# Kernel tuning notes

Hardware: AMD Instinct MI355X
Metric: run time of the kernel (lower is better)

The kernel has to match this reference:

```python
import jax, jax.numpy as jnp
import numpy as np

B0, L0, C0 = 4, 576, 256
DST, DCONV, EXP = 48, 4, 2
DIN = EXP * C0          # 512 internal dim
DTR = C0 // 16          # 16 delta rank
FD = 2 * C0             # 512 ffn dim (mlp_ratio=2)


def setup_inputs() -> dict:
    key = jax.random.key(0)
    ks = iter(jax.random.split(key, 32))
    def n(shape, s=0.02):
        return jax.random.normal(next(ks), shape, dtype=jnp.float32) * s
    return {
        'x': jax.random.normal(next(ks), (B0, L0, C0), dtype=jnp.float32),
        'ln1_g': jnp.ones((C0,), jnp.float32), 'ln1_b': jnp.zeros((C0,), jnp.float32),
        'mln_g': jnp.ones((C0,), jnp.float32), 'mln_b': jnp.zeros((C0,), jnp.float32),
        'w_in': n((C0, DIN * EXP)),
        'conv_w': n((DCONV, DIN)), 'conv_b': jnp.zeros((DIN,), jnp.float32),
        'w_xproj': n((DIN, DTR + 2 * DST)),
        'w_dt': n((DTR, DIN)), 'b_dt': jnp.zeros((DIN,), jnp.float32),
        'A_log': jnp.log(jnp.tile(jnp.arange(1, DST + 1, dtype=jnp.float32), (DIN, 1))),
        'D': jnp.ones((DIN,), jnp.float32),
        'w_out': n((DIN, C0)),
        'ln2_g': jnp.ones((C0,), jnp.float32), 'ln2_b': jnp.zeros((C0,), jnp.float32),
        'fc1_w': n((C0, FD)), 'bn1_s': jnp.ones((FD,), jnp.float32), 'bn1_b': jnp.zeros((FD,), jnp.float32),
        'Wr': n((FD, FD)), 'Wi': n((FD, FD)), 'rb': n((FD,)), 'ib': n((FD,)),
        'fc2_w': n((FD, C0)), 'bn2_s': jnp.ones((C0,), jnp.float32), 'bn2_b': jnp.zeros((C0,), jnp.float32),
    }


def _ln(x, g, b, eps=1e-3):
    m = jnp.mean(x, -1, keepdims=True)
    v = jnp.mean((x - m) ** 2, -1, keepdims=True)
    return (x - m) / jnp.sqrt(v + eps) * g + b


def _selective_scan(u, delta, A, Bm, Cm, D):
    # u,delta:[b,l,d]; A:[d,n]; Bm,Cm:[b,l,n]; D:[d]
    dA = jnp.einsum('bld,dn->bldn', delta, A)
    dB_u = jnp.einsum('bld,bld,bln->bldn', delta, u, Bm)
    shifted = jnp.pad(dA[:, 1:], ((0, 0), (1, 1), (0, 0), (0, 0)))[:, 1:]
    dA_cumsum = jnp.exp(jnp.cumsum(shifted[:, ::-1], axis=1))[:, ::-1]
    xs = jnp.cumsum(dB_u * dA_cumsum, axis=1) / (dA_cumsum + 1e-12)
    y = jnp.einsum('bldn,bln->bld', xs, Cm)
    return y + u * D


def _forward(x, ln1_g, ln1_b, mln_g, mln_b, w_in, conv_w, conv_b, w_xproj, w_dt, b_dt,
             A_log, D, w_out, ln2_g, ln2_b, fc1_w, bn1_s, bn1_b, Wr, Wi, rb, ib,
             fc2_w, bn2_s, bn2_b):
    # ---- Mamba branch: x + Mamba(LN_mamba(LN1(x))) ----
    h = _ln(_ln(x, ln1_g, ln1_b), mln_g, mln_b)
    xr = h @ w_in                                   # [b,l,4C]
    xm, res = xr[..., :DIN], xr[..., DIN:]
    # causal depthwise conv1d (pad left k-1)
    xp = jnp.pad(xm, ((0, 0), (DCONV - 1, 0), (0, 0)))
    xc = jax.lax.conv_general_dilated(
        xp, conv_w[:, None, :], (1,), 'VALID',
        dimension_numbers=('NLC', 'LIO', 'NLC'), feature_group_count=DIN) + conv_b
    xc = jax.nn.silu(xc)
    A = -jnp.exp(A_log)
    x_dbl = xc @ w_xproj
    dt, Bm, Cm = x_dbl[..., :DTR], x_dbl[..., DTR:DTR + DST], x_dbl[..., DTR + DST:]
    delta = jax.nn.softplus(dt @ w_dt + b_dt)
    y = _selective_scan(xc, delta, A, Bm, Cm, D)
    y = y * jax.nn.silu(res)
    x = x + y @ w_out
    # ---- Frequency-domain FFN branch: x + FFN(LN2(x)) ----
    h2 = _ln(x, ln2_g, ln2_b)
    f = jax.nn.relu((h2 @ fc1_w) * bn1_s + bn1_b)   # fc1 (1x1 conv) + BN(eval) + ReLU
    L = f.shape[1]
    scale = L ** 0.5
    fr = jnp.fft.rfft(f, axis=1)                    # fft over sequence length
    real, imag = fr.real / scale, fr.imag / scale
    xre = jax.nn.relu(jnp.einsum('bnc,cd->bnd', real, Wr) - jnp.einsum('bnc,cd->bnd', imag, Wi) + rb)
    xim = jax.nn.relu(jnp.einsum('bnc,cd->bnd', imag, Wr) + jnp.einsum('bnc,cd->bnd', real, Wi) + ib)
    ff = jnp.fft.irfft((xre + 1j * xim) * scale, n=L, axis=1)
    out2 = (ff @ fc2_w) * bn2_s + bn2_b             # fc2 (1x1 conv) + BN(eval)
    return x + out2


def reference(x, ln1_g, ln1_b, mln_g, mln_b, w_in, conv_w, conv_b, w_xproj, w_dt, b_dt,
              A_log, D, w_out, ln2_g, ln2_b, fc1_w, bn1_s, bn1_b, Wr, Wi, rb, ib,
              fc2_w, bn2_s, bn2_b):
    return _forward(x, ln1_g, ln1_b, mln_g, mln_b, w_in, conv_w, conv_b, w_xproj, w_dt,
                    b_dt, A_log, D, w_out, ln2_g, ln2_b, fc1_w, bn1_s, bn1_b, Wr, Wi,
                    rb, ib, fc2_w, bn2_s, bn2_b)
```

## Files before the change

kernel.cpp:

```cpp
#include <hip/hip_runtime.h>
#include <math.h>

#define NB 4
#define NL 576
#define NC 256
#define NTOK (NB*NL)
#define NDIN 512
#define NXD 112
#define NDTR 16
#define NDST 48
#define NFREQ 289
#define NWIN 1024
#define NMROW (NB*NFREQ)
#define NKPK 608

#define OFF_HB    0u
#define OFF_XRF   147456u
#define OFF_XCT   2506752u
#define OFF_REST  3686400u
#define OFF_XCB   4866048u
#define OFF_XDBL  5455872u
#define OFF_YFT   5584896u
#define OFF_X2    6764544u
#define OFF_FTB   7354368u
#define OFF_RF    7944192u
#define OFF_IF    8240128u
#define OFF_YFB   8536064u
#define OFF_FFB   9125888u
#define OFF_WINT  9715712u
#define OFF_WRT   9846784u
#define OFF_WIT   9977856u
#define OFF_WXPT  10108928u
#define OFF_WOT   10137600u
#define OFF_FC1T  10203136u
#define OFF_FC2T  10268672u
#define OFF_CF    10334208u
#define OFF_SF    10426368u
#define OFF_CI    10518528u

typedef __attribute__((ext_vector_type(8))) short bf16x8;
typedef __attribute__((ext_vector_type(4))) float f32x4;
typedef __attribute__((ext_vector_type(4))) int   i32x4;

__device__ __forceinline__ float wave_sum(float v) {
#pragma unroll
  for (int o = 32; o > 0; o >>= 1) v += __shfl_xor(v, o);
  return v;
}

__device__ __forceinline__ unsigned short f2bf(float f) {
  unsigned int u = __float_as_uint(f);
  unsigned int r = (u + 0x7fffu + ((u >> 16) & 1u)) >> 16;
  return (unsigned short)r;
}
__device__ __forceinline__ float b2f(unsigned short u) {
  return __uint_as_float(((unsigned int)u) << 16);
}

__device__ __forceinline__ float wave_iscan(float x, int lane) {
  x += __int_as_float(__builtin_amdgcn_update_dpp(0, __float_as_int(x), 0x111, 0xf, 0xf, true));
  x += __int_as_float(__builtin_amdgcn_update_dpp(0, __float_as_int(x), 0x112, 0xf, 0xf, true));
  x += __int_as_float(__builtin_amdgcn_update_dpp(0, __float_as_int(x), 0x114, 0xf, 0xf, true));
  x += __int_as_float(__builtin_amdgcn_update_dpp(0, __float_as_int(x), 0x118, 0xf, 0xf, true));
  int xi = __float_as_int(x);
  float s15 = __int_as_float(__builtin_amdgcn_readlane(xi, 15));
  float s31 = __int_as_float(__builtin_amdgcn_readlane(xi, 31));
  float s47 = __int_as_float(__builtin_amdgcn_readlane(xi, 47));
  float off = 0.f;
  if (lane >= 16) off += s15;
  if (lane >= 32) off += s31;
  if (lane >= 48) off += s47;
  return x + off;
}

__device__ void packT_dev(const float* __restrict__ src, unsigned short* __restrict__ dst,
                          int R, int C, int tile, int cblks) {
  __shared__ float t[64][65];
  int cb = tile % cblks, rb = tile / cblks;
  int c0 = cb * 64, r0 = rb * 64;
  int tid = threadIdx.x;
  for (int u = tid; u < 4096; u += 256) {
    int r = u >> 6, c = u & 63;
    float v = 0.f;
    if (r0 + r < R && c0 + c < C) v = src[(size_t)(r0 + r) * C + c0 + c];
    t[r][c] = v;
  }
  __syncthreads();
  for (int u = tid; u < 4096; u += 256) {
    int nr = u >> 6, nc = u & 63;
    if (c0 + nr < C && r0 + nc < R)
      dst[(size_t)(c0 + nr) * R + r0 + nc] = f2bf(t[nc][nr]);
  }
}

__global__ __launch_bounds__(256) void setup_kernel(
    const float* __restrict__ w_in, const float* __restrict__ Wr,
    const float* __restrict__ Wi, const float* __restrict__ wxp,
    const float* __restrict__ wo, const float* __restrict__ fc1,
    const float* __restrict__ fc2,
    unsigned short* __restrict__ winT, unsigned short* __restrict__ Wrt,
    unsigned short* __restrict__ Wit, unsigned short* __restrict__ wxpT,
    unsigned short* __restrict__ woT, unsigned short* __restrict__ fc1T,
    unsigned short* __restrict__ fc2T, unsigned short* __restrict__ Cf,
    unsigned short* __restrict__ Sf, unsigned short* __restrict__ Ci) {
  int bid = blockIdx.x;
  const float TWO_PI_N = 6.28318530717958647692f / (float)NL;
  if (bid < 64)       packT_dev(w_in, winT, NC, NWIN, bid, 16);
  else if (bid < 128) packT_dev(Wr, Wrt, NDIN, NDIN, bid - 64, 8);
  else if (bid < 192) packT_dev(Wi, Wit, NDIN, NDIN, bid - 128, 8);
  else if (bid < 208) packT_dev(wxp, wxpT, NDIN, NXD, bid - 192, 2);
  else if (bid < 240) packT_dev(wo, woT, NDIN, NC, bid - 208, 4);
  else if (bid < 272) packT_dev(fc1, fc1T, NC, NDIN, bid - 240, 8);
  else if (bid < 304) packT_dev(fc2, fc2T, NDIN, NC, bid - 272, 4);
  else if (bid < 384) {
    int m0 = (bid - 304) * 4;
    for (int u = threadIdx.x; u < 4 * NL; u += 256) {
      int m = m0 + u / NL, l = u % NL;
      float c = 0.f, s = 0.f;
      if (m < NFREQ) {
        int idx = (m * l) % NL;
        float sv, cv;
        __sincosf(TWO_PI_N * idx, &sv, &cv);
        c = cv * (1.f / 24.f);
        s = -sv * (1.f / 24.f);
      }
      Cf[(size_t)m * NL + l] = f2bf(c);
      Sf[(size_t)m * NL + l] = f2bf(s);
    }
  } else {
    int l0 = (bid - 384) * 8;
    for (int u = threadIdx.x; u < 8 * NKPK; u += 256) {
      int l = l0 + u / NKPK, k = u % NKPK;
      float v = 0.f;
      if (k < NFREQ) {
        float w = (k == 0 || k == NFREQ - 1) ? 1.f : 2.f;
        int idx = (k * l) % NL;
        float sv, cv;
        __sincosf(TWO_PI_N * idx, &sv, &cv);
        v = w * cv * (1.f / 24.f);
      } else if (k < 2 * NFREQ) {
        int kk = k - NFREQ;
        float w = (kk == 0 || kk == NFREQ - 1) ? 1.f : 2.f;
        int idx = (kk * l) % NL;
        float sv, cv;
        __sincosf(TWO_PI_N * idx, &sv, &cv);
        v = -w * sv * (1.f / 24.f);
      }
      Ci[(size_t)l * NKPK + k] = f2bf(v);
    }
  }
}

__global__ void ln_kernel(const float* __restrict__ in, unsigned short* __restrict__ out,
                          const float* __restrict__ g1, const float* __restrict__ b1,
                          const float* __restrict__ g2, const float* __restrict__ b2,
                          int dbl) {
  int row = blockIdx.x, lane = threadIdx.x;
  const float* p = in + (size_t)row * NC;
  float v[4];
#pragma unroll
  for (int j = 0; j < 4; ++j) v[j] = p[lane + j * 64];
  float s = wave_sum(v[0] + v[1] + v[2] + v[3]);
  float m = s * (1.f / NC);
  float q = 0.f;
#pragma unroll
  for (int j = 0; j < 4; ++j) { float d = v[j] - m; q += d * d; }
  q = wave_sum(q);
  float rs = 1.f / sqrtf(q * (1.f / NC) + 1e-3f);
#pragma unroll
  for (int j = 0; j < 4; ++j) {
    int c = lane + j * 64;
    v[j] = (v[j] - m) * rs * g1[c] + b1[c];
  }
  if (dbl) {
    s = wave_sum(v[0] + v[1] + v[2] + v[3]);
    m = s * (1.f / NC);
    q = 0.f;
#pragma unroll
    for (int j = 0; j < 4; ++j) { float d = v[j] - m; q += d * d; }
    q = wave_sum(q);
    rs = 1.f / sqrtf(q * (1.f / NC) + 1e-3f);
#pragma unroll
    for (int j = 0; j < 4; ++j) {
      int c = lane + j * 64;
      v[j] = (v[j] - m) * rs * g2[c] + b2[c];
    }
  }
  unsigned short* o = out + (size_t)row * NC;
#pragma unroll
  for (int j = 0; j < 4; ++j) o[lane + j * 64] = f2bf(v[j]);
}

__global__ __launch_bounds__(256) void packT_kernel(
    const float* __restrict__ src, unsigned short* __restrict__ dst, int R, int C) {
  packT_dev(src, dst, R, C, blockIdx.y * gridDim.x + blockIdx.x, gridDim.x);
}

__global__ __launch_bounds__(256) void gemm_mfma(
    const unsigned short* __restrict__ A, const unsigned short* __restrict__ B,
    void* __restrict__ C, int ldc, int M, int N, int K, int mode, int flags,
    const float* __restrict__ scl, const float* __restrict__ bias,
    const float* __restrict__ add, int ldadd) {
  __shared__ unsigned short As[64][40], Bs[64][40];
  int tid = threadIdx.x, lane = tid & 63, wv = tid >> 6;
  int n0 = blockIdx.x * 64, m0 = blockIdx.y * 64;
  int sm = tid >> 2, part = tid & 3;
  f32x4 acc[4] = {};
  for (int k0 = 0; k0 < K; k0 += 32) {
    *(bf16x8*)&As[sm][part * 8] = *(const bf16x8*)(A + (size_t)(m0 + sm) * K + k0 + part * 8);
    bf16x8 bv = {};
    if (n0 + sm < N) bv = *(const bf16x8*)(B + (size_t)(n0 + sm) * K + k0 + part * 8);
    *(bf16x8*)&Bs[sm][part * 8] = bv;
    __syncthreads();
    int am = wv * 16 + (lane & 15), koff = (lane >> 4) * 8;
    bf16x8 a = *(bf16x8*)&As[am][koff];
#pragma unroll
    for (int t = 0; t < 4; ++t) {
      bf16x8 b = *(bf16x8*)&Bs[t * 16 + (lane & 15)][koff];
      acc[t] = __builtin_amdgcn_mfma_f32_16x16x32_bf16(a, b, acc[t], 0, 0, 0);
    }
    __syncthreads();
  }
#pragma unroll
  for (int t = 0; t < 4; ++t) {
    int gn = n0 + t * 16 + (lane & 15);
    if (gn >= N) continue;
    float sv = scl ? scl[gn] : 0.f, bvv = bias ? bias[gn] : 0.f;
#pragma unroll
    for (int r = 0; r < 4; ++r) {
      int gm = m0 + wv * 16 + (lane >> 4) * 4 + r;
      float v = acc[t][r];
      if (mode == 2) v += add[(size_t)gm * ldadd + gn];
      else if (mode == 3) v = fmaxf(v * sv + bvv, 0.f);
      else if (mode == 4) v = v * sv + bvv + add[(size_t)gm * ldadd + gn];
      int gms = gm;
      if (flags & 8) {
        int bq = gm / NL, tt = gm - bq * NL;
        int t9 = tt / 9;
        gms = bq * NL + (tt - t9 * 9) * 64 + t9;
      }
      size_t o = (flags & 2) ? (size_t)gn * ldc + gms : (size_t)gm * ldc + gn;
      if (flags & 4) ((unsigned short*)C)[o] = f2bf(v);
      else ((float*)C)[o] = v;
    }
  }
}

__global__ __launch_bounds__(256) void convT_kernel(
    const float* __restrict__ xr, const float* __restrict__ cw,
    const float* __restrict__ cb, float* __restrict__ xc_t,
    float* __restrict__ res_t, unsigned short* __restrict__ xcb) {
  __shared__ float tile[67][65];
  int d0 = blockIdx.x * 64;
  int rt = blockIdx.y;
  int b = rt / 9, l0 = (rt % 9) * 64;
  int tid = threadIdx.x;
  int li = tid & 63, dj0 = tid >> 6;
  if (blockIdx.z == 0) {
    for (int u = tid; u < 67 * 16; u += 256) {
      int r = u >> 4, c4 = (u & 15) * 4;
      int l = l0 - 3 + r;
      float4 v = make_float4(0.f, 0.f, 0.f, 0.f);
      if (l >= 0) v = *reinterpret_cast<const float4*>(xr + (size_t)(b * NL + l) * NWIN + d0 + c4);
      tile[r][c4 + 0] = v.x; tile[r][c4 + 1] = v.y;
      tile[r][c4 + 2] = v.z; tile[r][c4 + 3] = v.w;
    }
    __syncthreads();
    float outv[16];
#pragma unroll
    for (int k2 = 0; k2 < 16; ++k2) {
      int dj = dj0 + k2 * 4;
      int d = d0 + dj;
      float acc = cb[d];
#pragma unroll
      for (int k = 0; k < 4; ++k) acc += cw[k * NDIN + d] * tile[li + k][dj];
      acc = acc / (1.f + __expf(-acc));
      outv[k2] = acc;
      xc_t[(size_t)d * NTOK + b * NL + l0 + li] = acc;
    }
    __syncthreads();
#pragma unroll
    for (int k2 = 0; k2 < 16; ++k2) tile[li][dj0 + k2 * 4] = outv[k2];
    __syncthreads();
    for (int u = tid; u < 1024; u += 256) {
      int r = u >> 4, c4 = (u & 15) * 4;
      unsigned long long pk =
          (unsigned long long)f2bf(tile[r][c4 + 0]) |
          ((unsigned long long)f2bf(tile[r][c4 + 1]) << 16) |
          ((unsigned long long)f2bf(tile[r][c4 + 2]) << 32) |
          ((unsigned long long)f2bf(tile[r][c4 + 3]) << 48);
      *(unsigned long long*)(xcb + (size_t)(b * NL + l0 + r) * NDIN + d0 + c4) = pk;
    }
  } else {
    for (int u = tid; u < 64 * 16; u += 256) {
      int r = u >> 4, c4 = (u & 15) * 4;
      float4 v = *reinterpret_cast<const float4*>(xr + (size_t)(b * NL + l0 + r) * NWIN + NDIN + d0 + c4);
      tile[r][c4 + 0] = v.x; tile[r][c4 + 1] = v.y;
      tile[r][c4 + 2] = v.z; tile[r][c4 + 3] = v.w;
    }
    __syncthreads();
    for (int dj = dj0; dj < 64; dj += 4)
      res_t[(size_t)(d0 + dj) * NTOK + b * NL + l0 + li] = tile[li][dj];
  }
}

__global__ __launch_bounds__(256) void scan7_kernel(
    const float* __restrict__ xc_t, const unsigned short* __restrict__ xdbl,
    const float* __restrict__ w_dt, const float* __restrict__ b_dt,
    const float* __restrict__ A_log, const float* __restrict__ Dp,
    const float* __restrict__ res_t, float* __restrict__ yf_t) {
  __shared__ float yl[4][NL];
  __shared__ float u_lds[NL];
  int b = blockIdx.x >> 9, d = blockIdx.x & 511;
  int tid = threadIdx.x, lane = tid & 63, wv = tid >> 6;
  int bbase = b * NL;
  const float* urow = xc_t + (size_t)d * NTOK;

  for (int e = tid; e < NL; e += 256) u_lds[e] = urow[bbase + e];

  float wdt[16];
#pragma unroll
  for (int r = 0; r < 16; ++r) wdt[r] = w_dt[r * NDIN + d];
  float bd = b_dt[d];
  float dl[9];
#pragma unroll
  for (int j = 0; j < 9; ++j) dl[j] = bd;
#pragma unroll
  for (int r = 0; r < 16; ++r) {
    const unsigned short* dtp = xdbl + (size_t)r * NTOK + bbase;
#pragma unroll
    for (int j = 0; j < 9; ++j) dl[j] += b2f(dtp[j * 64 + lane]) * wdt[r];
  }
#pragma unroll
  for (int j = 0; j < 9; ++j) {
    float v = dl[j];
    dl[j] = fmaxf(v, 0.f) + __logf(1.f + __expf(-fabsf(v)));
  }
  __syncthreads();

  float ul[9];
#pragma unroll
  for (int j = 0; j < 9; ++j) ul[j] = u_lds[lane * 9 + j];
  float pre[9];
  float s = 0.f;
#pragma unroll
  for (int j = 0; j < 9; ++j) { s += dl[j]; pre[j] = s; }
  float isc = wave_iscan(s, lane);
  float total = __int_as_float(__builtin_amdgcn_readlane(__float_as_int(isc), 63));
  float excl = isc - s;
  float Ts[9], dlul[9];
#pragma unroll
  for (int j = 0; j < 9; ++j) {
    Ts[j] = total - excl - pre[j];
    dlul[j] = dl[j] * ul[j];
  }

  const float* Arow = A_log + (size_t)d * NDST + wv * 12;
  float y[9] = {};
  for (int jj = 0; jj < 12; ++jj) {
    float An = -__expf(Arow[jj]);
    const unsigned short* bbp = xdbl + (size_t)(NDTR + wv * 12 + jj) * NTOK + bbase;
    const unsigned short* ccp = xdbl + (size_t)(NDTR + NDST + wv * 12 + jj) * NTOK + bbase;
    float e[9], w[9];
    float ps = 0.f;
#pragma unroll
    for (int j = 0; j < 9; ++j) {
      e[j] = __expf(An * Ts[j]);
      ps += dlul[j] * b2f(bbp[j * 64 + lane]) * e[j];
      w[j] = ps;
    }
    float wi = wave_iscan(ps, lane);
    float wexcl = wi - ps;
#pragma unroll
    for (int j = 0; j < 9; ++j)
      y[j] += __fdividef(w[j] + wexcl, e[j] + 1e-12f) * b2f(ccp[j * 64 + lane]);
  }
#pragma unroll
  for (int j = 0; j < 9; ++j) yl[wv][lane * 9 + j] = y[j];
  __syncthreads();

  const float* rrow = res_t + (size_t)d * NTOK;
  float* orow = yf_t + (size_t)d * NTOK;
  float Dd = Dp[d];
  for (int e0 = tid; e0 < NL; e0 += 256) {
    float yy = yl[0][e0] + yl[1][e0] + yl[2][e0] + yl[3][e0];
    float uu = u_lds[e0];
    float rr = rrow[bbase + e0];
    float yv = yy + uu * Dd;
    float sr = rr / (1.f + __expf(-rr));
    orow[bbase + e0] = yv * sr;
  }
}

__global__ __launch_bounds__(256) void dftf_mfma_kernel(
    const unsigned short* __restrict__ Cf, const unsigned short* __restrict__ Sf,
    const unsigned short* __restrict__ ft,
    unsigned short* __restrict__ RFb, unsigned short* __restrict__ IFb) {
  __shared__ unsigned short AsC[64][40], AsS[64][40], Bs[64][40];
  int tid = threadIdx.x;
  int lane = tid & 63, wv = tid >> 6;
  int n0 = blockIdx.x * 64, m0 = blockIdx.y * 64, b = blockIdx.z;
  int sm = tid >> 2, part = tid & 3;
  f32x4 accR[4] = {}, accI[4] = {};
  for (int k0 = 0; k0 < NL; k0 += 32) {
    *(bf16x8*)&AsC[sm][part * 8] = *(const bf16x8*)(Cf + (size_t)(m0 + sm) * NL + k0 + part * 8);
    *(bf16x8*)&AsS[sm][part * 8] = *(const bf16x8*)(Sf + (size_t)(m0 + sm) * NL + k0 + part * 8);
    *(bf16x8*)&Bs[sm][part * 8]  = *(const bf16x8*)(ft + (size_t)(n0 + sm) * NTOK + b * NL + k0 + part * 8);
    __syncthreads();
    int am = wv * 16 + (lane & 15);
    int koff = (lane >> 4) * 8;
    bf16x8 ac = *(bf16x8*)&AsC[am][koff];
    bf16x8 as = *(bf16x8*)&AsS[am][koff];
#pragma unroll
    for (int t = 0; t < 4; ++t) {
      bf16x8 bv = *(bf16x8*)&Bs[t * 16 + (lane & 15)][koff];
      accR[t] = __builtin_amdgcn_mfma_f32_16x16x32_bf16(ac, bv, accR[t], 0, 0, 0);
      accI[t] = __builtin_amdgcn_mfma_f32_16x16x32_bf16(as, bv, accI[t], 0, 0, 0);
    }
    __syncthreads();
  }
#pragma unroll
  for (int t = 0; t < 4; ++t) {
    int gn = n0 + t * 16 + (lane & 15);
#pragma unroll
    for (int r = 0; r < 4; ++r) {
      int gm = m0 + wv * 16 + (lane >> 4) * 4 + r;
      if (gm < NFREQ) {
        size_t o = ((size_t)(b * NFREQ + gm)) * NDIN + gn;
        RFb[o] = f2bf(accR[t][r]);
        IFb[o] = f2bf(accI[t][r]);
      }
    }
  }
}

__global__ __launch_bounds__(256) void mix_mfma_kernel(
    const unsigned short* __restrict__ RFb, const unsigned short* __restrict__ IFb,
    const unsigned short* __restrict__ Wrt, const unsigned short* __restrict__ Wit,
    const float* __restrict__ rb, const float* __restrict__ ib,
    unsigned short* __restrict__ PK) {
  __shared__ unsigned short AsR[64][40], AsI[64][40], BsR[64][40], BsI[64][40];
  int tid = threadIdx.x;
  int lane = tid & 63, wv = tid >> 6;
  int n0 = blockIdx.x * 64, m0 = blockIdx.y * 64;
  int sm = tid >> 2, part = tid & 3;
  f32x4 accR[4] = {}, accI[4] = {};
  for (int k0 = 0; k0 < NDIN; k0 += 32) {
    *(bf16x8*)&AsR[sm][part * 8] = *(const bf16x8*)(Wrt + (size_t)(m0 + sm) * NDIN + k0 + part * 8);
    *(bf16x8*)&AsI[sm][part * 8] = *(const bf16x8*)(Wit + (size_t)(m0 + sm) * NDIN + k0 + part * 8);
    bf16x8 brf = {}, bif = {};
    if (n0 + sm < NMROW) {
      brf = *(const bf16x8*)(RFb + (size_t)(n0 + sm) * NDIN + k0 + part * 8);
      bif = *(const bf16x8*)(IFb + (size_t)(n0 + sm) * NDIN + k0 + part * 8);
    }
    *(bf16x8*)&BsR[sm][part * 8] = brf;
    *(bf16x8*)&BsI[sm][part * 8] = bif;
    __syncthreads();
    int am = wv * 16 + (lane & 15);
    int koff = (lane >> 4) * 8;
    bf16x8 a_wr = *(bf16x8*)&AsR[am][koff];
    bf16x8 a_wi = *(bf16x8*)&AsI[am][koff];
    union { bf16x8 h; i32x4 i; } un;
    un.h = a_wi;
    un.i = un.i ^ (int)0x80008000;
    bf16x8 a_win = un.h;
#pragma unroll
    for (int t = 0; t < 4; ++t) {
      bf16x8 b_rf = *(bf16x8*)&BsR[t * 16 + (lane & 15)][koff];
      bf16x8 b_if = *(bf16x8*)&BsI[t * 16 + (lane & 15)][koff];
      accR[t] = __builtin_amdgcn_mfma_f32_16x16x32_bf16(a_wr, b_rf, accR[t], 0, 0, 0);
      accR[t] = __builtin_amdgcn_mfma_f32_16x16x32_bf16(a_win, b_if, accR[t], 0, 0, 0);
      accI[t] = __builtin_amdgcn_mfma_f32_16x16x32_bf16(a_wr, b_if, accI[t], 0, 0, 0);
      accI[t] = __builtin_amdgcn_mfma_f32_16x16x32_bf16(a_wi, b_rf, accI[t], 0, 0, 0);
    }
    __syncthreads();
  }
#pragma unroll
  for (int t = 0; t < 4; ++t) {
    int gn = n0 + t * 16 + (lane & 15);
    int bb = (gn >= 3 * NFREQ) ? 3 : (gn >= 2 * NFREQ) ? 2 : (gn >= NFREQ) ? 1 : 0;
    int kf = gn - bb * NFREQ;
    bool ok = gn < NMROW;
#pragma unroll
    for (int r = 0; r < 4; ++r) {
      int gm = m0 + wv * 16 + (lane >> 4) * 4 + r;
      if (ok) {
        float vr = fmaxf(accR[t][r] + rb[gm], 0.f);
        float vi = fmaxf(accI[t][r] + ib[gm], 0.f);
        size_t base = ((size_t)gm * NB + bb) * NKPK;
        PK[base + kf] = f2bf(vr);
        PK[base + NFREQ + kf] = f2bf(vi);
      }
    }
  }
}

__global__ __launch_bounds__(256) void idft_mfma_kernel(
    const unsigned short* __restrict__ Ci, const unsigned short* __restrict__ PK,
    unsigned short* __restrict__ ffb) {
  __shared__ unsigned short As[64][40], Bs[64][40];
  int tid = threadIdx.x;
  int lane = tid & 63, wv = tid >> 6;
  int n0 = blockIdx.x * 64, m0 = blockIdx.y * 64, b = blockIdx.z;
  int sm = tid >> 2, part = tid & 3;
  f32x4 acc[4] = {};
  for (int k0 = 0; k0 < NKPK; k0 += 32) {
    *(bf16x8*)&As[sm][part * 8] = *(const bf16x8*)(Ci + (size_t)(m0 + sm) * NKPK + k0 + part * 8);
    bf16x8 bv = *(const bf16x8*)(PK + ((size_t)(n0 + sm) * NB + b) * NKPK + k0 + part * 8);
    if (k0 + part * 8 >= 2 * NFREQ - 2) {
      union { bf16x8 h; i32x4 i; } u;
      u.h = bv;
      if (k0 + part * 8 == 576) { u.i[1] = 0; u.i[2] = 0; u.i[3] = 0; }
      else { u.i[0] = 0; u.i[1] = 0; u.i[2] = 0; u.i[3] = 0; }
      bv = u.h;
    }
    *(bf16x8*)&Bs[sm][part * 8] = bv;
    __syncthreads();
    int am = wv * 16 + (lane & 15);
    int koff = (lane >> 4) * 8;
    bf16x8 av = *(bf16x8*)&As[am][koff];
#pragma unroll
    for (int t = 0; t < 4; ++t) {
      bf16x8 b2 = *(bf16x8*)&Bs[t * 16 + (lane & 15)][koff];
      acc[t] = __builtin_amdgcn_mfma_f32_16x16x32_bf16(av, b2, acc[t], 0, 0, 0);
    }
    __syncthreads();
  }
#pragma unroll
  for (int t = 0; t < 4; ++t) {
    int gn = n0 + t * 16 + (lane & 15);
#pragma unroll
    for (int r = 0; r < 4; ++r) {
      int gm = m0 + wv * 16 + (lane >> 4) * 4 + r;
      ffb[((size_t)(b * NL + gm)) * NDIN + gn] = f2bf(acc[t][r]);
    }
  }
}

extern "C" void kernel_launch(void* const* d_in, const int* in_sizes, int n_in,
                              void* d_out, int out_size, void* d_ws, size_t ws_size,
                              hipStream_t stream) {
  const float* x      = (const float*)d_in[0];
  const float* ln1_g  = (const float*)d_in[1];
  const float* ln1_b  = (const float*)d_in[2];
  const float* mln_g  = (const float*)d_in[3];
  const float* mln_b  = (const float*)d_in[4];
  const float* w_in   = (const float*)d_in[5];
  const float* conv_w = (const float*)d_in[6];
  const float* conv_b = (const float*)d_in[7];
  const float* w_xprj = (const float*)d_in[8];
  const float* w_dt   = (const float*)d_in[9];
  const float* b_dt   = (const float*)d_in[10];
  const float* A_log  = (const float*)d_in[11];
  const float* Dp     = (const float*)d_in[12];
  const float* w_out  = (const float*)d_in[13];
  const float* ln2_g  = (const float*)d_in[14];
  const float* ln2_b  = (const float*)d_in[15];
  const float* fc1_w  = (const float*)d_in[16];
  const float* bn1_s  = (const float*)d_in[17];
  const float* bn1_b  = (const float*)d_in[18];
  const float* Wr     = (const float*)d_in[19];
  const float* Wi     = (const float*)d_in[20];
  const float* rb     = (const float*)d_in[21];
  const float* ib     = (const float*)d_in[22];
  const float* fc2_w  = (const float*)d_in[23];
  const float* bn2_s  = (const float*)d_in[24];
  const float* bn2_b  = (const float*)d_in[25];

  float* ws = (float*)d_ws;
  unsigned short* hb   = (unsigned short*)(ws + OFF_HB);
  float* xr     = ws + OFF_XRF;
  float* xc_t   = ws + OFF_XCT;
  float* res_t  = ws + OFF_REST;
  float* yf_t   = ws + OFF_YFT;
  float* x2     = ws + OFF_X2;
  unsigned short* xcb  = (unsigned short*)(ws + OFF_XCB);
  unsigned short* xdbl = (unsigned short*)(ws + OFF_XDBL);
  unsigned short* PK   = (unsigned short*)(ws + OFF_YFT);
  unsigned short* ftb  = (unsigned short*)(ws + OFF_FTB);
  unsigned short* RFb  = (unsigned short*)(ws + OFF_RF);
  unsigned short* IFb  = (unsigned short*)(ws + OFF_IF);
  unsigned short* yfb  = (unsigned short*)(ws + OFF_YFB);
  unsigned short* ffb  = (unsigned short*)(ws + OFF_FFB);
  unsigned short* winT = (unsigned short*)(ws + OFF_WINT);
  unsigned short* Wrt  = (unsigned short*)(ws + OFF_WRT);
  unsigned short* Wit  = (unsigned short*)(ws + OFF_WIT);
  unsigned short* wxpT = (unsigned short*)(ws + OFF_WXPT);
  unsigned short* woT  = (unsigned short*)(ws + OFF_WOT);
  unsigned short* fc1T = (unsigned short*)(ws + OFF_FC1T);
  unsigned short* fc2T = (unsigned short*)(ws + OFF_FC2T);
  unsigned short* Cfb  = (unsigned short*)(ws + OFF_CF);
  unsigned short* Sfb  = (unsigned short*)(ws + OFF_SF);
  unsigned short* Cib  = (unsigned short*)(ws + OFF_CI);
  unsigned short* h2b  = hb;
  float* out = (float*)d_out;

  setup_kernel<<<456, 256, 0, stream>>>(w_in, Wr, Wi, w_xprj, w_out, fc1_w, fc2_w,
                                        winT, Wrt, Wit, wxpT, woT, fc1T, fc2T,
                                        Cfb, Sfb, Cib);
  ln_kernel<<<NTOK, 64, 0, stream>>>(x, hb, ln1_g, ln1_b, mln_g, mln_b, 1);
  gemm_mfma<<<dim3(16, 36), 256, 0, stream>>>(hb, winT, xr, NWIN, NTOK, NWIN, NC,
                                              0, 0, nullptr, nullptr, nullptr, 0);
  convT_kernel<<<dim3(8, 36, 2), 256, 0, stream>>>(xr, conv_w, conv_b, xc_t, res_t, xcb);
  gemm_mfma<<<dim3(2, 36), 256, 0, stream>>>(xcb, wxpT, xdbl, NTOK, NTOK, NXD, NDIN,
                                             0, 14, nullptr, nullptr, nullptr, 0);
  scan7_kernel<<<NB * NDIN, 256, 0, stream>>>(xc_t, xdbl, w_dt, b_dt, A_log, Dp, res_t, yf_t);
  packT_kernel<<<dim3(36, 8), 256, 0, stream>>>(yf_t, yfb, NDIN, NTOK);
  gemm_mfma<<<dim3(4, 36), 256, 0, stream>>>(yfb, woT, x2, NC, NTOK, NC, NDIN,
                                             2, 0, nullptr, nullptr, x, NC);
  ln_kernel<<<NTOK, 64, 0, stream>>>(x2, h2b, ln2_g, ln2_b, nullptr, nullptr, 0);
  gemm_mfma<<<dim3(8, 36), 256, 0, stream>>>(h2b, fc1T, ftb, NTOK, NTOK, NDIN, NC,
                                             3, 6, bn1_s, bn1_b, nullptr, 0);
  dftf_mfma_kernel<<<dim3(8, 5, NB), 256, 0, stream>>>(Cfb, Sfb, ftb, RFb, IFb);
  mix_mfma_kernel<<<dim3(19, 8), 256, 0, stream>>>(RFb, IFb, Wrt, Wit, rb, ib, PK);
  idft_mfma_kernel<<<dim3(8, 9, NB), 256, 0, stream>>>(Cib, PK, ffb);
  gemm_mfma<<<dim3(4, 36), 256, 0, stream>>>(ffb, fc2T, out, NC, NTOK, NC, NDIN,
                                             4, 0, bn2_s, bn2_b, x2, NC);
}
```

Before: 186.2 us.

## Store in-proj, conv and residual intermediates as bf16 and restructure scan

The in-projection GEMM now writes bf16 output, and the conv/transposition kernel reads bf16 and writes the transposed conv activations and residual as bf16. This roughly halves the memory traffic of these intermediates between the GEMM, conv and scan kernels. The scan kernel computes delta cooperatively into shared memory across all threads instead of redundantly per wave. It also processes two state channels per iteration to expose more independent exp and scan work. The cost is reduced precision on u and the residual gate, plus extra shared memory and register pressure.

After: 199.9 us. 1.07x slower.

```diff
diff --git a/kernel.cpp b/kernel.cpp
--- a/kernel.cpp
+++ b/kernel.cpp
@@ -247,9 +247,9 @@
 }
 
 __global__ __launch_bounds__(256) void convT_kernel(
-    const float* __restrict__ xr, const float* __restrict__ cw,
-    const float* __restrict__ cb, float* __restrict__ xc_t,
-    float* __restrict__ res_t, unsigned short* __restrict__ xcb) {
+    const unsigned short* __restrict__ xrb, const float* __restrict__ cw,
+    const float* __restrict__ cb, unsigned short* __restrict__ xc_tb,
+    unsigned short* __restrict__ res_tb, unsigned short* __restrict__ xcb) {
   __shared__ float tile[67][65];
   int d0 = blockIdx.x * 64;
   int rt = blockIdx.y;
@@ -257,13 +257,17 @@
   int tid = threadIdx.x;
   int li = tid & 63, dj0 = tid >> 6;
   if (blockIdx.z == 0) {
-    for (int u = tid; u < 67 * 16; u += 256) {
-      int r = u >> 4, c4 = (u & 15) * 4;
+    for (int u = tid; u < 67 * 8; u += 256) {
+      int r = u >> 3, c8 = (u & 7) * 8;
       int l = l0 - 3 + r;
-      float4 v = make_float4(0.f, 0.f, 0.f, 0.f);
-      if (l >= 0) v = *reinterpret_cast<const float4*>(xr + (size_t)(b * NL + l) * NWIN + d0 + c4);
-      tile[r][c4 + 0] = v.x; tile[r][c4 + 1] = v.y;
-      tile[r][c4 + 2] = v.z; tile[r][c4 + 3] = v.w;
+      if (l >= 0) {
+        bf16x8 v = *(const bf16x8*)(xrb + (size_t)(b * NL + l) * NWIN + d0 + c8);
+#pragma unroll
+        for (int q = 0; q < 8; ++q) tile[r][c8 + q] = b2f((unsigned short)v[q]);
+      } else {
+#pragma unroll
+        for (int q = 0; q < 8; ++q) tile[r][c8 + q] = 0.f;
+      }
     }
     __syncthreads();
     float outv[16];
@@ -276,7 +280,7 @@
       for (int k = 0; k < 4; ++k) acc += cw[k * NDIN + d] * tile[li + k][dj];
       acc = acc / (1.f + __expf(-acc));
       outv[k2] = acc;
-      xc_t[(size_t)d * NTOK + b * NL + l0 + li] = acc;
+      xc_tb[(size_t)d * NTOK + b * NL + l0 + li] = f2bf(acc);
     }
     __syncthreads();
 #pragma unroll
@@ -292,55 +296,50 @@
       *(unsigned long long*)(xcb + (size_t)(b * NL + l0 + r) * NDIN + d0 + c4) = pk;
     }
   } else {
-    for (int u = tid; u < 64 * 16; u += 256) {
-      int r = u >> 4, c4 = (u & 15) * 4;
-      float4 v = *reinterpret_cast<const float4*>(xr + (size_t)(b * NL + l0 + r) * NWIN + NDIN + d0 + c4);
-      tile[r][c4 + 0] = v.x; tile[r][c4 + 1] = v.y;
-      tile[r][c4 + 2] = v.z; tile[r][c4 + 3] = v.w;
+    for (int u = tid; u < 64 * 8; u += 256) {
+      int r = u >> 3, c8 = (u & 7) * 8;
+      bf16x8 v = *(const bf16x8*)(xrb + (size_t)(b * NL + l0 + r) * NWIN + NDIN + d0 + c8);
+#pragma unroll
+      for (int q = 0; q < 8; ++q) tile[r][c8 + q] = b2f((unsigned short)v[q]);
     }
     __syncthreads();
     for (int dj = dj0; dj < 64; dj += 4)
-      res_t[(size_t)(d0 + dj) * NTOK + b * NL + l0 + li] = tile[li][dj];
-  }
-}
-
-__global__ __launch_bounds__(256) void scan7_kernel(
-    const float* __restrict__ xc_t, const unsigned short* __restrict__ xdbl,
+      res_tb[(size_t)(d0 + dj) * NTOK + b * NL + l0 + li] = f2bf(tile[li][dj]);
+  }
+}
+
+__global__ __launch_bounds__(256) void scan8_kernel(
+    const unsigned short* __restrict__ xc_tb, const unsigned short* __restrict__ xdbl,
     const float* __restrict__ w_dt, const float* __restrict__ b_dt,
     const float* __restrict__ A_log, const float* __restrict__ Dp,
-    const float* __restrict__ res_t, float* __restrict__ yf_t) {
+    const unsigned short* __restrict__ res_tb, float* __restrict__ yf_t) {
   __shared__ float yl[4][NL];
   __shared__ float u_lds[NL];
+  __shared__ float dl_lds[NL];
   int b = blockIdx.x >> 9, d = blockIdx.x & 511;
   int tid = threadIdx.x, lane = tid & 63, wv = tid >> 6;
   int bbase = b * NL;
-  const float* urow = xc_t + (size_t)d * NTOK;
-
-  for (int e = tid; e < NL; e += 256) u_lds[e] = urow[bbase + e];
-
+  const unsigned short* urow = xc_tb + (size_t)d * NTOK;
+
+  for (int e = tid; e < NL; e += 256) u_lds[e] = b2f(urow[bbase + e]);
   float wdt[16];
 #pragma unroll
   for (int r = 0; r < 16; ++r) wdt[r] = w_dt[r * NDIN + d];
   float bd = b_dt[d];
-  float dl[9];
-#pragma unroll
-  for (int j = 0; j < 9; ++j) dl[j] = bd;
-#pragma unroll
-  for (int r = 0; r < 16; ++r) {
-    const unsigned short* dtp = xdbl + (size_t)r * NTOK + bbase;
-#pragma unroll
-    for (int j = 0; j < 9; ++j) dl[j] += b2f(dtp[j * 64 + lane]) * wdt[r];
-  }
+  for (int p = tid; p < NL; p += 256) {
+    float v = bd;
+#pragma unroll
+    for (int r = 0; r < 16; ++r) v += b2f(xdbl[(size_t)r * NTOK + bbase + p]) * wdt[r];
+    dl_lds[p] = fmaxf(v, 0.f) + __logf(1.f + __expf(-fabsf(v)));
+  }
+  __syncthreads();
+
+  float dl[9], ul[9];
 #pragma unroll
   for (int j = 0; j < 9; ++j) {
-    float v = dl[j];
-    dl[j] = fmaxf(v, 0.f) + __logf(1.f + __expf(-fabsf(v)));
-  }
-  __syncthreads();
-
-  float ul[9];
-#pragma unroll
-  for (int j = 0; j < 9; ++j) ul[j] = u_lds[lane * 9 + j];
+    dl[j] = dl_lds[j * 64 + lane];
+    ul[j] = u_lds[lane * 9 + j];
+  }
   float pre[9];
   float s = 0.f;
 #pragma unroll
@@ -357,38 +356,47 @@
 
   const float* Arow = A_log + (size_t)d * NDST + wv * 12;
   float y[9] = {};
-  for (int jj = 0; jj < 12; ++jj) {
-    float An = -__expf(Arow[jj]);
-    const unsigned short* bbp = xdbl + (size_t)(NDTR + wv * 12 + jj) * NTOK + bbase;
-    const unsigned short* ccp = xdbl + (size_t)(NDTR + NDST + wv * 12 + jj) * NTOK + bbase;
-    float e[9], w[9];
-    float ps = 0.f;
+  for (int jj = 0; jj < 12; jj += 2) {
+    float An0 = -__expf(Arow[jj]);
+    float An1 = -__expf(Arow[jj + 1]);
+    const unsigned short* bbp0 = xdbl + (size_t)(NDTR + wv * 12 + jj) * NTOK + bbase;
+    const unsigned short* ccp0 = xdbl + (size_t)(NDTR + NDST + wv * 12 + jj) * NTOK + bbase;
+    const unsigned short* bbp1 = bbp0 + NTOK;
+    const unsigned short* ccp1 = ccp0 + NTOK;
+    float e0[9], e1[9], w0[9], w1[9];
+    float ps0 = 0.f, ps1 = 0.f;
 #pragma unroll
     for (int j = 0; j < 9; ++j) {
-      e[j] = __expf(An * Ts[j]);
-      ps += dlul[j] * b2f(bbp[j * 64 + lane]) * e[j];
-      w[j] = ps;
-    }
-    float wi = wave_iscan(ps, lane);
-    float wexcl = wi - ps;
-#pragma unroll
-    for (int j = 0; j < 9; ++j)
-      y[j] += __fdividef(w[j] + wexcl, e[j] + 1e-12f) * b2f(ccp[j * 64 + lane]);
+      e0[j] = __expf(An0 * Ts[j]);
+      e1[j] = __expf(An1 * Ts[j]);
+      ps0 += dlul[j] * b2f(bbp0[j * 64 + lane]) * e0[j];
+      ps1 += dlul[j] * b2f(bbp1[j * 64 + lane]) * e1[j];
+      w0[j] = ps0;
+      w1[j] = ps1;
+    }
+    float wi0 = wave_iscan(ps0, lane);
+    float wi1 = wave_iscan(ps1, lane);
+    float we0 = wi0 - ps0, we1 = wi1 - ps1;
+#pragma unroll
+    for (int j = 0; j < 9; ++j) {
+      y[j] += __fdividef(w0[j] + we0, e0[j] + 1e-12f) * b2f(ccp0[j * 64 + lane]);
+      y[j] += __fdividef(w1[j] + we1, e1[j] + 1e-12f) * b2f(ccp1[j * 64 + lane]);
+    }
   }
 #pragma unroll
   for (int j = 0; j < 9; ++j) yl[wv][lane * 9 + j] = y[j];
   __syncthreads();
 
-  const float* rrow = res_t + (size_t)d * NTOK;
+  const unsigned short* rrow = res_tb + (size_t)d * NTOK;
   float* orow = yf_t + (size_t)d * NTOK;
   float Dd = Dp[d];
-  for (int e0 = tid; e0 < NL; e0 += 256) {
-    float yy = yl[0][e0] + yl[1][e0] + yl[2][e0] + yl[3][e0];
-    float uu = u_lds[e0];
-    float rr = rrow[bbase + e0];
+  for (int e0i = tid; e0i < NL; e0i += 256) {
+    float yy = yl[0][e0i] + yl[1][e0i] + yl[2][e0i] + yl[3][e0i];
+    float uu = u_lds[e0i];
+    float rr = b2f(rrow[bbase + e0i]);
     float yv = yy + uu * Dd;
     float sr = rr / (1.f + __expf(-rr));
-    orow[bbase + e0] = yv * sr;
+    orow[bbase + e0i] = yv * sr;
   }
 }
 
@@ -568,10 +576,10 @@
   const float* bn2_b  = (const float*)d_in[25];
 
   float* ws = (float*)d_ws;
-  unsigned short* hb   = (unsigned short*)(ws + OFF_HB);
-  float* xr     = ws + OFF_XRF;
-  float* xc_t   = ws + OFF_XCT;
-  float* res_t  = ws + OFF_REST;
+  unsigned short* hb    = (unsigned short*)(ws + OFF_HB);
+  unsigned short* xrb   = (unsigned short*)(ws + OFF_XRF);
+  unsigned short* xc_tb = (unsigned short*)(ws + OFF_XCT);
+  unsigned short* res_tb= (unsigned short*)(ws + OFF_REST);
   float* yf_t   = ws + OFF_YFT;
   float* x2     = ws + OFF_X2;
   unsigned short* xcb  = (unsigned short*)(ws + OFF_XCB);
@@ -599,12 +607,12 @@
                                         winT, Wrt, Wit, wxpT, woT, fc1T, fc2T,
                                         Cfb, Sfb, Cib);
   ln_kernel<<<NTOK, 64, 0, stream>>>(x, hb, ln1_g, ln1_b, mln_g, mln_b, 1);
-  gemm_mfma<<<dim3(16, 36), 256, 0, stream>>>(hb, winT, xr, NWIN, NTOK, NWIN, NC,
-                                              0, 0, nullptr, nullptr, nullptr, 0);
-  convT_kernel<<<dim3(8, 36, 2), 256, 0, stream>>>(xr, conv_w, conv_b, xc_t, res_t, xcb);
+  gemm_mfma<<<dim3(16, 36), 256, 0, stream>>>(hb, winT, xrb, NWIN, NTOK, NWIN, NC,
+                                              0, 4, nullptr, nullptr, nullptr, 0);
+  convT_kernel<<<dim3(8, 36, 2), 256, 0, stream>>>(xrb, conv_w, conv_b, xc_tb, res_tb, xcb);
   gemm_mfma<<<dim3(2, 36), 256, 0, stream>>>(xcb, wxpT, xdbl, NTOK, NTOK, NXD, NDIN,
                                              0, 14, nullptr, nullptr, nullptr, 0);
-  scan7_kernel<<<NB * NDIN, 256, 0, stream>>>(xc_t, xdbl, w_dt, b_dt, A_log, Dp, res_t, yf_t);
+  scan8_kernel<<<NB * NDIN, 256, 0, stream>>>(xc_tb, xdbl, w_dt, b_dt, A_log, Dp, res_tb, yf_t);
   packT_kernel<<<dim3(36, 8), 256, 0, stream>>>(yf_t, yfb, NDIN, NTOK);
   gemm_mfma<<<dim3(4, 36), 256, 0, stream>>>(yfb, woT, x2, NC, NTOK, NC, NDIN,
                                              2, 0, nullptr, nullptr, x, NC);
```

## Fuse first LayerNorm into setup kernel and pack x_proj output pairwise for scan

Applied to the files above, without the earlier changes.

The double LayerNorm on the input moves into extra blocks of the setup kernel, which removes one kernel launch. The x_proj GEMM epilogue now writes its bf16 output in an interleaved layout: delta-rank channels are paired, and each B channel sits next to its matching C channel. The scan can then fetch two values with one 32-bit load. The scan also switches from exp to exp2 with the log2(e) factor pre-multiplied. The risks are scattered 2-byte stores in the GEMM epilogue and a larger setup grid.

New measurement: 187.5 us. No clear change (+0.7%).

```diff
diff --git a/kernel.cpp b/kernel.cpp
--- a/kernel.cpp
+++ b/kernel.cpp
@@ -93,6 +93,41 @@
   }
 }
 
+__device__ void ln_row2(const float* __restrict__ in, unsigned short* __restrict__ out,
+                        const float* __restrict__ g1, const float* __restrict__ b1,
+                        const float* __restrict__ g2, const float* __restrict__ b2,
+                        int row, int lane) {
+  const float* p = in + (size_t)row * NC;
+  float v[4];
+#pragma unroll
+  for (int j = 0; j < 4; ++j) v[j] = p[lane + j * 64];
+  float s = wave_sum(v[0] + v[1] + v[2] + v[3]);
+  float m = s * (1.f / NC);
+  float q = 0.f;
+#pragma unroll
+  for (int j = 0; j < 4; ++j) { float dd = v[j] - m; q += dd * dd; }
+  q = wave_sum(q);
+  float rs = 1.f / sqrtf(q * (1.f / NC) + 1e-3f);
+#pragma unroll
+  for (int j = 0; j < 4; ++j) {
+    int c = lane + j * 64;
+    v[j] = (v[j] - m) * rs * g1[c] + b1[c];
+  }
+  s = wave_sum(v[0] + v[1] + v[2] + v[3]);
+  m = s * (1.f / NC);
+  q = 0.f;
+#pragma unroll
+  for (int j = 0; j < 4; ++j) { float dd = v[j] - m; q += dd * dd; }
+  q = wave_sum(q);
+  rs = 1.f / sqrtf(q * (1.f / NC) + 1e-3f);
+  unsigned short* o = out + (size_t)row * NC;
+#pragma unroll
+  for (int j = 0; j < 4; ++j) {
+    int c = lane + j * 64;
+    o[c] = f2bf((v[j] - m) * rs * g2[c] + b2[c]);
+  }
+}
+
 __global__ __launch_bounds__(256) void setup_kernel(
     const float* __restrict__ w_in, const float* __restrict__ Wr,
     const float* __restrict__ Wi, const float* __restrict__ wxp,
@@ -102,7 +137,10 @@
     unsigned short* __restrict__ Wit, unsigned short* __restrict__ wxpT,
     unsigned short* __restrict__ woT, unsigned short* __restrict__ fc1T,
     unsigned short* __restrict__ fc2T, unsigned short* __restrict__ Cf,
-    unsigned short* __restrict__ Sf, unsigned short* __restrict__ Ci) {
+    unsigned short* __restrict__ Sf, unsigned short* __restrict__ Ci,
+    const float* __restrict__ x, unsigned short* __restrict__ hb,
+    const float* __restrict__ ln1_g, const float* __restrict__ ln1_b,
+    const float* __restrict__ mln_g, const float* __restrict__ mln_b) {
   int bid = blockIdx.x;
   const float TWO_PI_N = 6.28318530717958647692f / (float)NL;
   if (bid < 64)       packT_dev(w_in, winT, NC, NWIN, bid, 16);
@@ -127,7 +165,7 @@
       Cf[(size_t)m * NL + l] = f2bf(c);
       Sf[(size_t)m * NL + l] = f2bf(s);
     }
-  } else {
+  } else if (bid < 456) {
     int l0 = (bid - 384) * 8;
     for (int u = threadIdx.x; u < 8 * NKPK; u += 256) {
       int l = l0 + u / NKPK, k = u % NKPK;
@@ -148,13 +186,14 @@
       }
       Ci[(size_t)l * NKPK + k] = f2bf(v);
     }
+  } else {
+    int row = (bid - 456) * 4 + (threadIdx.x >> 6);
+    ln_row2(x, hb, ln1_g, ln1_b, mln_g, mln_b, row, threadIdx.x & 63);
   }
 }
 
 __global__ void ln_kernel(const float* __restrict__ in, unsigned short* __restrict__ out,
-                          const float* __restrict__ g1, const float* __restrict__ b1,
-                          const float* __restrict__ g2, const float* __restrict__ b2,
-                          int dbl) {
+                          const float* __restrict__ g1, const float* __restrict__ b1) {
   int row = blockIdx.x, lane = threadIdx.x;
   const float* p = in + (size_t)row * NC;
   float v[4];
@@ -167,28 +206,12 @@
   for (int j = 0; j < 4; ++j) { float d = v[j] - m; q += d * d; }
   q = wave_sum(q);
   float rs = 1.f / sqrtf(q * (1.f / NC) + 1e-3f);
+  unsigned short* o = out + (size_t)row * NC;
 #pragma unroll
   for (int j = 0; j < 4; ++j) {
     int c = lane + j * 64;
-    v[j] = (v[j] - m) * rs * g1[c] + b1[c];
-  }
-  if (dbl) {
-    s = wave_sum(v[0] + v[1] + v[2] + v[3]);
-    m = s * (1.f / NC);
-    q = 0.f;
-#pragma unroll
-    for (int j = 0; j < 4; ++j) { float d = v[j] - m; q += d * d; }
-    q = wave_sum(q);
-    rs = 1.f / sqrtf(q * (1.f / NC) + 1e-3f);
-#pragma unroll
-    for (int j = 0; j < 4; ++j) {
-      int c = lane + j * 64;
-      v[j] = (v[j] - m) * rs * g2[c] + b2[c];
-    }
-  }
-  unsigned short* o = out + (size_t)row * NC;
-#pragma unroll
-  for (int j = 0; j < 4; ++j) o[lane + j * 64] = f2bf(v[j]);
+    o[c] = f2bf((v[j] - m) * rs * g1[c] + b1[c]);
+  }
 }
 
 __global__ __launch_bounds__(256) void packT_kernel(
@@ -233,6 +256,18 @@
       if (mode == 2) v += add[(size_t)gm * ldadd + gn];
       else if (mode == 3) v = fmaxf(v * sv + bvv, 0.f);
       else if (mode == 4) v = v * sv + bvv + add[(size_t)gm * ldadd + gn];
+      if (flags & 16) {
+        int bq = gm / NL, tt = gm - bq * NL;
+        int t9 = tt / 9;
+        int pt = bq * NL + (tt - t9 * 9) * 64 + t9;
+        unsigned short* D = (unsigned short*)C;
+        size_t idx;
+        if (gn < NDTR) idx = (((size_t)(gn >> 1)) * NTOK + pt) * 2 + (gn & 1);
+        else if (gn < NDTR + NDST) idx = (size_t)16 * NTOK + ((size_t)(gn - NDTR) * NTOK + pt) * 2;
+        else idx = (size_t)16 * NTOK + ((size_t)(gn - NDTR - NDST) * NTOK + pt) * 2 + 1;
+        D[idx] = f2bf(v);
+        continue;
+      }
       int gms = gm;
       if (flags & 8) {
         int bq = gm / NL, tt = gm - bq * NL;
@@ -304,8 +339,8 @@
   }
 }
 
-__global__ __launch_bounds__(256) void scan7_kernel(
-    const float* __restrict__ xc_t, const unsigned short* __restrict__ xdbl,
+__global__ __launch_bounds__(256) void scan9_kernel(
+    const float* __restrict__ xc_t, const unsigned int* __restrict__ xdp,
     const float* __restrict__ w_dt, const float* __restrict__ b_dt,
     const float* __restrict__ A_log, const float* __restrict__ Dp,
     const float* __restrict__ res_t, float* __restrict__ yf_t) {
@@ -321,15 +356,18 @@
   float wdt[16];
 #pragma unroll
   for (int r = 0; r < 16; ++r) wdt[r] = w_dt[r * NDIN + d];
-  float bd = b_dt[d];
   float dl[9];
 #pragma unroll
-  for (int j = 0; j < 9; ++j) dl[j] = bd;
-#pragma unroll
-  for (int r = 0; r < 16; ++r) {
-    const unsigned short* dtp = xdbl + (size_t)r * NTOK + bbase;
-#pragma unroll
-    for (int j = 0; j < 9; ++j) dl[j] += b2f(dtp[j * 64 + lane]) * wdt[r];
+  for (int j = 0; j < 9; ++j) dl[j] = b_dt[d];
+#pragma unroll
+  for (int pr = 0; pr < 8; ++pr) {
+    const unsigned int* p = xdp + (size_t)pr * NTOK + bbase;
+    float w0 = wdt[2 * pr], w1 = wdt[2 * pr + 1];
+#pragma unroll
+    for (int j = 0; j < 9; ++j) {
+      unsigned int u = p[j * 64 + lane];
+      dl[j] += b2f((unsigned short)u) * w0 + b2f((unsigned short)(u >> 16)) * w1;
+    }
   }
 #pragma unroll
   for (int j = 0; j < 9; ++j) {
@@ -356,24 +394,26 @@
   }
 
   const float* Arow = A_log + (size_t)d * NDST + wv * 12;
+  const unsigned int* bcP = xdp + (size_t)8 * NTOK;
   float y[9] = {};
   for (int jj = 0; jj < 12; ++jj) {
-    float An = -__expf(Arow[jj]);
-    const unsigned short* bbp = xdbl + (size_t)(NDTR + wv * 12 + jj) * NTOK + bbase;
-    const unsigned short* ccp = xdbl + (size_t)(NDTR + NDST + wv * 12 + jj) * NTOK + bbase;
+    float An2 = -__expf(Arow[jj]) * 1.44269504088896f;
+    const unsigned int* p = bcP + (size_t)(wv * 12 + jj) * NTOK + bbase;
+    unsigned int bc[9];
     float e[9], w[9];
     float ps = 0.f;
 #pragma unroll
     for (int j = 0; j < 9; ++j) {
-      e[j] = __expf(An * Ts[j]);
-      ps += dlul[j] * b2f(bbp[j * 64 + lane]) * e[j];
+      bc[j] = p[j * 64 + lane];
+      e[j] = exp2f(An2 * Ts[j]);
+      ps += dlul[j] * b2f((unsigned short)bc[j]) * e[j];
       w[j] = ps;
     }
     float wi = wave_iscan(ps, lane);
     float wexcl = wi - ps;
 #pragma unroll
     for (int j = 0; j < 9; ++j)
-      y[j] += __fdividef(w[j] + wexcl, e[j] + 1e-12f) * b2f(ccp[j * 64 + lane]);
+      y[j] += __fdividef(w[j] + wexcl, e[j] + 1e-12f) * b2f((unsigned short)(bc[j] >> 16));
   }
 #pragma unroll
   for (int j = 0; j < 9; ++j) yl[wv][lane * 9 + j] = y[j];
@@ -575,7 +615,7 @@
   float* yf_t   = ws + OFF_YFT;
   float* x2     = ws + OFF_X2;
   unsigned short* xcb  = (unsigned short*)(ws + OFF_XCB);
-  unsigned short* xdbl = (unsigned short*)(ws + OFF_XDBL);
+  unsigned int*   xdp  = (unsigned int*)(ws + OFF_XDBL);
   unsigned short* PK   = (unsigned short*)(ws + OFF_YFT);
   unsigned short* ftb  = (unsigned short*)(ws + OFF_FTB);
   unsigned short* RFb  = (unsigned short*)(ws + OFF_RF);
@@ -595,20 +635,20 @@
   unsigned short* h2b  = hb;
   float* out = (float*)d_out;
 
-  setup_kernel<<<456, 256, 0, stream>>>(w_in, Wr, Wi, w_xprj, w_out, fc1_w, fc2_w,
-                                        winT, Wrt, Wit, wxpT, woT, fc1T, fc2T,
-                                        Cfb, Sfb, Cib);
-  ln_kernel<<<NTOK, 64, 0, stream>>>(x, hb, ln1_g, ln1_b, mln_g, mln_b, 1);
+  setup_kernel<<<1032, 256, 0, stream>>>(w_in, Wr, Wi, w_xprj, w_out, fc1_w, fc2_w,
+                                         winT, Wrt, Wit, wxpT, woT, fc1T, fc2T,
+                                         Cfb, Sfb, Cib,
+                                         x, hb, ln1_g, ln1_b, mln_g, mln_b);
   gemm_mfma<<<dim3(16, 36), 256, 0, stream>>>(hb, winT, xr, NWIN, NTOK, NWIN, NC,
                                               0, 0, nullptr, nullptr, nullptr, 0);
   convT_kernel<<<dim3(8, 36, 2), 256, 0, stream>>>(xr, conv_w, conv_b, xc_t, res_t, xcb);
-  gemm_mfma<<<dim3(2, 36), 256, 0, stream>>>(xcb, wxpT, xdbl, NTOK, NTOK, NXD, NDIN,
-                                             0, 14, nullptr, nullptr, nullptr, 0);
-  scan7_kernel<<<NB * NDIN, 256, 0, stream>>>(xc_t, xdbl, w_dt, b_dt, A_log, Dp, res_t, yf_t);
+  gemm_mfma<<<dim3(2, 36), 256, 0, stream>>>(xcb, wxpT, xdp, NTOK, NTOK, NXD, NDIN,
+                                             0, 16, nullptr, nullptr, nullptr, 0);
+  scan9_kernel<<<NB * NDIN, 256, 0, stream>>>(xc_t, xdp, w_dt, b_dt, A_log, Dp, res_t, yf_t);
   packT_kernel<<<dim3(36, 8), 256, 0, stream>>>(yf_t, yfb, NDIN, NTOK);
   gemm_mfma<<<dim3(4, 36), 256, 0, stream>>>(yfb, woT, x2, NC, NTOK, NC, NDIN,
                                              2, 0, nullptr, nullptr, x, NC);
-  ln_kernel<<<NTOK, 64, 0, stream>>>(x2, h2b, ln2_g, ln2_b, nullptr, nullptr, 0);
+  ln_kernel<<<NTOK, 64, 0, stream>>>(x2, h2b, ln2_g, ln2_b);
   gemm_mfma<<<dim3(8, 36), 256, 0, stream>>>(h2b, fc1T, ftb, NTOK, NTOK, NDIN, NC,
                                              3, 6, bn1_s, bn1_b, nullptr, 0);
   dftf_mfma_kernel<<<dim3(8, 5, NB), 256, 0, stream>>>(Cfb, Sfb, ftb, RFb, IFb);
```
